# Optimization experiments

Measured on AMD Instinct MI355X. Metric: run time of the kernel, lower is better.

The kernel has to match this reference:

```python
import jax, jax.numpy as jnp
import numpy as np

B, S, H = 2, 2048, 4096
NH, HD = 32, 128  # n_heads, head_dim


def setup_inputs() -> dict:
    key = jax.random.key(0)
    ks = jax.random.split(key, 6)
    hidden_states = jax.random.normal(ks[0], (B, S, H), dtype=jnp.float32)
    alibi = jax.random.normal(ks[1], (B, NH, 1, S), dtype=jnp.float32)
    w_qkv = jax.random.normal(ks[2], (H, NH, 3 * HD), dtype=jnp.float32) * 0.02
    b_qkv = jax.random.normal(ks[3], (NH, 3 * HD), dtype=jnp.float32) * 0.02
    w_out = jax.random.normal(ks[4], (NH, HD, H), dtype=jnp.float32) * 0.02
    b_out = jax.random.normal(ks[5], (H,), dtype=jnp.float32) * 0.02
    attention_mask = jnp.ones((B, S), dtype=jnp.int32)
    return {"hidden_states": hidden_states, "alibi": alibi, "w_qkv": w_qkv,
            "b_qkv": b_qkv, "w_out": w_out, "b_out": b_out,
            "attention_mask": attention_mask}


def reference(hidden_states, alibi, w_qkv, b_qkv, w_out, b_out, attention_mask):
    dtype = hidden_states.dtype
    b, s, _ = hidden_states.shape
    # fused QKV projection: [b, s, heads, 3*head_dim]
    fused_qkv = jnp.einsum('bse,ehf->bshf', hidden_states, w_qkv) + b_qkv
    query, key, value = jnp.split(fused_qkv, 3, axis=-1)  # each [b, s, h, d]
    # causal mask fused with padding mask -> [b, 1, q, k] bool
    causal = jnp.tril(jnp.ones((s, s), dtype=bool))[None, None]
    pad = (attention_mask > 0)[:, None, None, :]
    mask = causal & pad
    mask_value = jnp.finfo(dtype).min
    attention_bias = jnp.where(mask, jnp.zeros((), dtype), jnp.full((), mask_value, dtype))
    attention_bias = attention_bias + alibi  # broadcast [b,1,q,k]+[b,h,1,k] -> [b,h,q,k]
    # scaled dot-product attention weights (query scaled by 1/sqrt(head_dim))
    scale = jnp.asarray(1.0 / np.sqrt(HD), dtype)
    scores = jnp.einsum('bqhd,bkhd->bhqk', query * scale, key) + attention_bias
    attn_weights = jax.nn.softmax(scores, axis=-1)
    attn_output = jnp.einsum('bhqk,bkhd->bqhd', attn_weights, value)
    # output projection contracting (heads, head_dim)
    out = jnp.einsum('bqhd,hde->bqe', attn_output, w_out) + b_out
    return out
```

## Files before the change

kernel.cpp:

```cpp
#include <hip/hip_runtime.h>
#include <math.h>

typedef __attribute__((ext_vector_type(8))) short bf16x8;
typedef __attribute__((ext_vector_type(4))) float f32x4;

#define MFMA16(a, b, c) __builtin_amdgcn_mfma_f32_16x16x32_bf16(a, b, c, 0, 0, 0)

#define GLD_LDS16(g, l)                                                          \
    __builtin_amdgcn_global_load_lds(                                            \
        (const __attribute__((address_space(1))) unsigned int*)(g),              \
        (__attribute__((address_space(3))) unsigned int*)(l), 16, 0, 0)

__device__ __forceinline__ short f2bf(float f) {
    union { float f; unsigned int u; } v; v.f = f;
    unsigned int u = v.u;
    u += 0x7FFFu + ((u >> 16) & 1u);
    return (short)(u >> 16);
}

__device__ __forceinline__ short f2bf_trunc(float f) {
    union { float f; unsigned int u; } v; v.f = f;
    return (short)(v.u >> 16);
}

__device__ __forceinline__ float fexp2(float x) {
#if __has_builtin(__builtin_amdgcn_exp2f)
    return __builtin_amdgcn_exp2f(x);
#else
    return __expf(x * 0.6931471805599453f);
#endif
}

__global__ __launch_bounds__(256) void cvt_kernel(const float* __restrict__ src,
                                                  short* __restrict__ dst, int n4) {
    int i = blockIdx.x * 256 + threadIdx.x;
    if (i >= n4) return;
    float4 v = ((const float4*)src)[i];
    short4 o;
    o.x = f2bf(v.x); o.y = f2bf(v.y); o.z = f2bf(v.z); o.w = f2bf(v.w);
    ((short4*)dst)[i] = o;
}

__global__ __launch_bounds__(256) void bias_prep_kernel(const float* __restrict__ alibi,
                                                        const int* __restrict__ amask,
                                                        float* __restrict__ cb) {
    int i = blockIdx.x * 256 + threadIdx.x;
    int bh = i >> 11, k = i & 2047;
    int b = bh >> 5;
    cb[i] = (amask[b * 2048 + k] > 0) ? alibi[i] * 1.4426950408889634f : -3.0e38f;
}

__global__ __launch_bounds__(256) void transpose_cvt_kernel(const float* __restrict__ src,
                                                            short* __restrict__ dst,
                                                            int R, int C) {
    __shared__ short tile[32][33];
    const int t = threadIdx.x;
    const int r0 = blockIdx.y << 5, c0 = blockIdx.x << 5;
    {
        int tr = t >> 3, tc = (t & 7) << 2;
        float4 v = *(const float4*)(src + (size_t)(r0 + tr) * C + c0 + tc);
        tile[tr][tc + 0] = f2bf(v.x);
        tile[tr][tc + 1] = f2bf(v.y);
        tile[tr][tc + 2] = f2bf(v.z);
        tile[tr][tc + 3] = f2bf(v.w);
    }
    __syncthreads();
    {
        int on = t >> 3, ok = (t & 7) << 2;
        short4 o;
        o.x = tile[ok + 0][on]; o.y = tile[ok + 1][on];
        o.z = tile[ok + 2][on]; o.w = tile[ok + 3][on];
        *(short4*)(dst + (size_t)(c0 + on) * R + r0 + ok) = o;
    }
}

__global__ __launch_bounds__(256) void qkv_gemm_kernel(const short* __restrict__ A,
                                                       const short* __restrict__ Bt,
                                                       const float* __restrict__ bias,
                                                       short* __restrict__ Qo,
                                                       short* __restrict__ Ko,
                                                       short* __restrict__ Vo) {
    const int K = 4096;
    __shared__ short As[128][32];
    __shared__ short Bs[128][32];
    const int t = threadIdx.x;
    const int m0 = blockIdx.x << 7;
    const int n0 = blockIdx.y << 7;
    const int lane = t & 63;
    const int w = t >> 6;
    const int l16 = lane & 15;
    const int quad = lane >> 4;
    const int wm = (w >> 1) << 6;
    const int wn = (w & 1) << 6;

    const int srow0 = (w << 5) + (lane >> 2);
    const int srow1 = srow0 + 16;
    const int scol = (lane & 3) << 3;

    f32x4 acc[4][4];
#pragma unroll
    for (int i = 0; i < 4; ++i)
#pragma unroll
        for (int j = 0; j < 4; ++j) acc[i][j] = (f32x4){0.f, 0.f, 0.f, 0.f};

    for (int k0 = 0; k0 < K; k0 += 32) {
        __syncthreads();
        GLD_LDS16(A + (size_t)(m0 + srow0) * K + k0 + scol, &As[srow0 & ~15][0]);
        GLD_LDS16(A + (size_t)(m0 + srow1) * K + k0 + scol, &As[srow1 & ~15][0]);
        GLD_LDS16(Bt + (size_t)(n0 + srow0) * K + k0 + scol, &Bs[srow0 & ~15][0]);
        GLD_LDS16(Bt + (size_t)(n0 + srow1) * K + k0 + scol, &Bs[srow1 & ~15][0]);
        __syncthreads();
        bf16x8 af[4], bfr[4];
#pragma unroll
        for (int mb = 0; mb < 4; ++mb)
            af[mb] = *(const bf16x8*)&As[wm + (mb << 4) + l16][quad << 3];
#pragma unroll
        for (int nb = 0; nb < 4; ++nb)
            bfr[nb] = *(const bf16x8*)&Bs[wn + (nb << 4) + l16][quad << 3];
#pragma unroll
        for (int mb = 0; mb < 4; ++mb)
#pragma unroll
            for (int nb = 0; nb < 4; ++nb)
                acc[mb][nb] = MFMA16(af[mb], bfr[nb], acc[mb][nb]);
    }

    const float qscale = 0.12751740806338946f;
#pragma unroll
    for (int nb = 0; nb < 4; ++nb) {
        int gn = n0 + wn + (nb << 4) + l16;
        float bv = bias[gn];
        int head = gn / 384, f = gn - head * 384;
#pragma unroll
        for (int mb = 0; mb < 4; ++mb) {
#pragma unroll
            for (int r = 0; r < 4; ++r) {
                int gm = m0 + wm + (mb << 4) + (quad << 2) + r;
                float v = acc[mb][nb][r] + bv;
                int b = gm >> 11, s = gm & 2047;
                int bhh = (b << 5) + head;
                if (f < 128) {
                    Qo[((size_t)bhh * 2048 + s) * 128 + f] = f2bf(v * qscale);
                } else if (f < 256) {
                    Ko[((size_t)bhh * 2048 + s) * 128 + (f - 128)] = f2bf(v);
                } else {
                    Vo[((size_t)bhh * 128 + (f - 256)) * 2048 + s] = f2bf(v);
                }
            }
        }
    }
}

__global__ __launch_bounds__(256) void out_gemm_kernel(const short* __restrict__ A,
                                                       const short* __restrict__ Bt,
                                                       const float* __restrict__ bias,
                                                       float* __restrict__ Co) {
    const int K = 4096, N = 4096;
    __shared__ short As[128][32];
    __shared__ short Bs[128][32];
    const int t = threadIdx.x;
    const int m0 = blockIdx.x << 7;
    const int n0 = blockIdx.y << 7;
    const int lane = t & 63;
    const int w = t >> 6;
    const int l16 = lane & 15;
    const int quad = lane >> 4;
    const int wm = (w >> 1) << 6;
    const int wn = (w & 1) << 6;

    const int srow0 = (w << 5) + (lane >> 2);
    const int srow1 = srow0 + 16;
    const int scol = (lane & 3) << 3;

    f32x4 acc[4][4];
#pragma unroll
    for (int i = 0; i < 4; ++i)
#pragma unroll
        for (int j = 0; j < 4; ++j) acc[i][j] = (f32x4){0.f, 0.f, 0.f, 0.f};

    for (int k0 = 0; k0 < K; k0 += 32) {
        __syncthreads();
        GLD_LDS16(A + (size_t)(m0 + srow0) * K + k0 + scol, &As[srow0 & ~15][0]);
        GLD_LDS16(A + (size_t)(m0 + srow1) * K + k0 + scol, &As[srow1 & ~15][0]);
        GLD_LDS16(Bt + (size_t)(n0 + srow0) * K + k0 + scol, &Bs[srow0 & ~15][0]);
        GLD_LDS16(Bt + (size_t)(n0 + srow1) * K + k0 + scol, &Bs[srow1 & ~15][0]);
        __syncthreads();
        bf16x8 af[4], bfr[4];
#pragma unroll
        for (int mb = 0; mb < 4; ++mb)
            af[mb] = *(const bf16x8*)&As[wm + (mb << 4) + l16][quad << 3];
#pragma unroll
        for (int nb = 0; nb < 4; ++nb)
            bfr[nb] = *(const bf16x8*)&Bs[wn + (nb << 4) + l16][quad << 3];
#pragma unroll
        for (int mb = 0; mb < 4; ++mb)
#pragma unroll
            for (int nb = 0; nb < 4; ++nb)
                acc[mb][nb] = MFMA16(af[mb], bfr[nb], acc[mb][nb]);
    }

#pragma unroll
    for (int nb = 0; nb < 4; ++nb) {
        int gn = n0 + wn + (nb << 4) + l16;
        float bv = bias[gn];
#pragma unroll
        for (int mb = 0; mb < 4; ++mb) {
#pragma unroll
            for (int r = 0; r < 4; ++r) {
                int gm = m0 + wm + (mb << 4) + (quad << 2) + r;
                Co[(size_t)gm * N + gn] = acc[mb][nb][r] + bv;
            }
        }
    }
}

__global__ __launch_bounds__(256) void attn_kernel(const short* __restrict__ Q,
                                                   const short* __restrict__ Kt,
                                                   const short* __restrict__ Vt,
                                                   const float* __restrict__ cbias,
                                                   short* __restrict__ Ot) {
    __shared__ short Ks[64][132];
    __shared__ short Vs[144][68];
    __shared__ short Ps[4][16][68];
    const int t = threadIdx.x;
    const int w = t >> 6;
    const int lane = t & 63;
    const int l16 = lane & 15;
    const int quad = lane >> 4;
    const int qt = 31 - blockIdx.x;
    const int bh = blockIdx.y;
    const int b = bh >> 5;
    const int h = bh & 31;
    const int q0t = qt << 6;

    const short* Qp = Q + (size_t)bh * 2048 * 128;
    const short* Kp = Kt + (size_t)bh * 2048 * 128;
    const short* Vp = Vt + (size_t)bh * 128 * 2048;
    const float* cb = cbias + (size_t)bh * 2048;

    const int kr = t >> 4, kc = (t & 15) << 3;
    const int vr = t >> 3, vc = (t & 7) << 3;

    for (int idx = t; idx < 16 * 68; idx += 256) {
        int rr = idx / 68, cc = idx - rr * 68;
        Vs[128 + rr][cc] = (rr == 0 && cc < 64) ? (short)0x3F80 : (short)0;
    }

    bf16x8 aq[4];
    const int myq = q0t + (w << 4) + l16;
#pragma unroll
    for (int kd = 0; kd < 4; ++kd)
        aq[kd] = *(const bf16x8*)(Qp + (size_t)myq * 128 + (kd << 5) + (quad << 3));

    f32x4 acc[9];
#pragma unroll
    for (int c = 0; c < 9; ++c) acc[c] = (f32x4){0.f, 0.f, 0.f, 0.f};
    float mrow[4];
#pragma unroll
    for (int r = 0; r < 4; ++r) mrow[r] = -3.0e38f;

    const int ktiles = qt + 1;

    bf16x8 Kreg[4], Vreg[4];
#pragma unroll
    for (int i = 0; i < 4; ++i) {
        Kreg[i] = *(const bf16x8*)(Kp + (size_t)(kr + (i << 4)) * 128 + kc);
        Vreg[i] = *(const bf16x8*)(Vp + (size_t)(vr + (i << 5)) * 2048 + vc);
    }

    for (int kt = 0; kt < ktiles; ++kt) {
        const int kk = kt << 6;
        __syncthreads();
#pragma unroll
        for (int i = 0; i < 4; ++i) {
            *(bf16x8*)&Ks[kr + (i << 4)][kc] = Kreg[i];
            *(bf16x8*)&Vs[vr + (i << 5)][vc] = Vreg[i];
        }
        if (kt + 1 < ktiles) {
            const int nk = kk + 64;
#pragma unroll
            for (int i = 0; i < 4; ++i) {
                Kreg[i] = *(const bf16x8*)(Kp + (size_t)(nk + kr + (i << 4)) * 128 + kc);
                Vreg[i] = *(const bf16x8*)(Vp + (size_t)(vr + (i << 5)) * 2048 + nk + vc);
            }
        }
        __syncthreads();

        float biasv[4];
#pragma unroll
        for (int j = 0; j < 4; ++j)
            biasv[j] = cb[kk + (j << 4) + l16];

        f32x4 sf[4];
#pragma unroll
        for (int nb = 0; nb < 4; ++nb) {
            sf[nb] = (f32x4){0.f, 0.f, 0.f, 0.f};
#pragma unroll
            for (int kd = 0; kd < 4; ++kd) {
                bf16x8 bk = *(const bf16x8*)&Ks[(nb << 4) + l16][(kd << 5) + (quad << 3)];
                sf[nb] = MFMA16(aq[kd], bk, sf[nb]);
            }
        }

        const int qrb = q0t + (w << 4) + (quad << 2);
        const bool diag = (kt == ktiles - 1);
        float alpha[4];
#pragma unroll
        for (int r = 0; r < 4; ++r) {
            float s[4];
#pragma unroll
            for (int j = 0; j < 4; ++j) s[j] = sf[j][r] + biasv[j];
            if (diag) {
                int qr = qrb + r;
#pragma unroll
                for (int j = 0; j < 4; ++j)
                    if (kk + (j << 4) + l16 > qr) s[j] = -3.0e38f;
            }
            float mx = fmaxf(fmaxf(s[0], s[1]), fmaxf(s[2], s[3]));
            mx = fmaxf(mx, __shfl_xor(mx, 1));
            mx = fmaxf(mx, __shfl_xor(mx, 2));
            mx = fmaxf(mx, __shfl_xor(mx, 4));
            mx = fmaxf(mx, __shfl_xor(mx, 8));
            float mnew = fmaxf(mrow[r], mx);
            alpha[r] = fexp2(mrow[r] - mnew);
            mrow[r] = mnew;
            int pq = (quad << 2) + r;
#pragma unroll
            for (int j = 0; j < 4; ++j)
                Ps[w][pq][(j << 4) + l16] = f2bf_trunc(fexp2(s[j] - mnew));
        }

        bf16x8 ap0 = *(const bf16x8*)&Ps[w][l16][quad << 3];
        bf16x8 ap1 = *(const bf16x8*)&Ps[w][l16][32 + (quad << 3)];
#pragma unroll
        for (int c = 0; c < 9; ++c) {
            bf16x8 bv0 = *(const bf16x8*)&Vs[(c << 4) + l16][quad << 3];
            bf16x8 bv1 = *(const bf16x8*)&Vs[(c << 4) + l16][32 + (quad << 3)];
            f32x4 ac = acc[c];
            ac[0] *= alpha[0]; ac[1] *= alpha[1]; ac[2] *= alpha[2]; ac[3] *= alpha[3];
            ac = MFMA16(ap0, bv0, ac);
            acc[c] = MFMA16(ap1, bv1, ac);
        }
    }

    float inv[4];
#pragma unroll
    for (int r = 0; r < 4; ++r) {
        float l = __shfl(acc[8][r], quad << 4);
        inv[r] = (l > 0.f) ? 1.0f / l : 0.f;
    }
    const int qbase = q0t + (w << 4) + (quad << 2);
#pragma unroll
    for (int c = 0; c < 8; ++c) {
        int d = (c << 4) + l16;
#pragma unroll
        for (int r = 0; r < 4; ++r) {
            int q = qbase + r;
            Ot[(size_t)(b * 2048 + q) * 4096 + h * 128 + d] = f2bf(acc[c][r] * inv[r]);
        }
    }
}

extern "C" void kernel_launch(void* const* d_in, const int* in_sizes, int n_in,
                              void* d_out, int out_size, void* d_ws, size_t ws_size,
                              hipStream_t stream) {
    const float* hidden = (const float*)d_in[0];
    const float* alibi  = (const float*)d_in[1];
    const float* w_qkv  = (const float*)d_in[2];
    const float* b_qkv  = (const float*)d_in[3];
    const float* w_out  = (const float*)d_in[4];
    const float* b_out  = (const float*)d_in[5];
    const int*   amask  = (const int*)d_in[6];
    float* out = (float*)d_out;

    char* ws = (char*)d_ws;
    short* hid_bf = (short*)(ws);
    short* wqkv_t = (short*)(ws + 33554432ull);
    short* wout_t = wqkv_t;
    float* cbias  = (float*)(ws + 67108864ull);
    short* Qb     = (short*)(ws + 134217728ull);
    short* Kb     = (short*)(ws + 167772160ull);
    short* Vb     = (short*)(ws + 201326592ull);
    short* attn_o = hid_bf;

    cvt_kernel<<<16384, 256, 0, stream>>>(hidden, hid_bf, 4194304);
    transpose_cvt_kernel<<<dim3(384, 128), 256, 0, stream>>>(w_qkv, wqkv_t, 4096, 12288);
    qkv_gemm_kernel<<<dim3(32, 96), 256, 0, stream>>>(hid_bf, wqkv_t, b_qkv, Qb, Kb, Vb);
    bias_prep_kernel<<<512, 256, 0, stream>>>(alibi, amask, cbias);
    transpose_cvt_kernel<<<dim3(128, 128), 256, 0, stream>>>(w_out, wout_t, 4096, 4096);
    attn_kernel<<<dim3(32, 64), 256, 0, stream>>>(Qb, Kb, Vb, cbias, attn_o);
    out_gemm_kernel<<<dim3(32, 32), 256, 0, stream>>>(attn_o, wout_t, b_out, out);
}
```

Measured before the change: 1.386 ms.

## Rewrite QKV and output GEMMs with 256x256 tiles and 4-stage LDS pipeline

Both projection GEMMs move from 128x128 tiles with 256 threads and single-buffered LDS to 256x256 tiles with 512 threads, 8 waves in a 2x4 arrangement. They also gain a 4-deep ring of global-to-LDS async loads with explicit vmcnt waits and split barriers. The LDS layout is XOR-swizzled to avoid bank conflicts, and MFMA blocks are wrapped in setprio. The goal is to hide global load latency, raise arithmetic intensity per block, and cut the two syncthreads per k-step. The cost is much higher register use (128 accumulator floats per lane), 128KB of LDS per block, and fewer blocks in flight (768 and 256).

```diff
diff --git a/kernel.cpp b/kernel.cpp
--- a/kernel.cpp
+++ b/kernel.cpp
@@ -74,68 +74,105 @@
     }
 }
 
-__global__ __launch_bounds__(256) void qkv_gemm_kernel(const short* __restrict__ A,
-                                                       const short* __restrict__ Bt,
-                                                       const float* __restrict__ bias,
-                                                       short* __restrict__ Qo,
-                                                       short* __restrict__ Ko,
-                                                       short* __restrict__ Vo) {
-    const int K = 4096;
-    __shared__ short As[128][32];
-    __shared__ short Bs[128][32];
+__global__ __launch_bounds__(512, 2) void qkv_gemm_kernel(const short* __restrict__ A,
+                                                          const short* __restrict__ Bt,
+                                                          const float* __restrict__ bias,
+                                                          short* __restrict__ Qo,
+                                                          short* __restrict__ Ko,
+                                                          short* __restrict__ Vo) {
+    __shared__ __attribute__((aligned(16))) short Al[4][8192];
+    __shared__ __attribute__((aligned(16))) short Bl[4][8192];
     const int t = threadIdx.x;
-    const int m0 = blockIdx.x << 7;
-    const int n0 = blockIdx.y << 7;
     const int lane = t & 63;
     const int w = t >> 6;
+    const int wm = w >> 2;
+    const int wn = w & 3;
     const int l16 = lane & 15;
     const int quad = lane >> 4;
-    const int wm = (w >> 1) << 6;
-    const int wn = (w & 1) << 6;
-
-    const int srow0 = (w << 5) + (lane >> 2);
-    const int srow1 = srow0 + 16;
-    const int scol = (lane & 3) << 3;
-
-    f32x4 acc[4][4];
-#pragma unroll
-    for (int i = 0; i < 4; ++i)
+    const int m0 = blockIdx.x << 8;
+    const int n0 = blockIdx.y << 8;
+
+    const int srow = lane >> 2;
+    const int skoff = (((lane & 3) ^ ((lane >> 3) & 3)) << 3);
+    const short* pA0 = A + (size_t)(m0 + (w << 5) + srow) * 4096 + skoff;
+    const short* pA1 = pA0 + (size_t)16 * 4096;
+    const short* pB0 = Bt + (size_t)(n0 + (w << 5) + srow) * 4096 + skoff;
+    const short* pB1 = pB0 + (size_t)16 * 4096;
+
+    const int qs = quad ^ ((l16 >> 1) & 3);
+    const int aoff = ((wm << 7) + l16) * 32 + (qs << 3);
+    const int boff = ((wn << 6) + l16) * 32 + (qs << 3);
+
+    f32x4 acc[8][4];
+#pragma unroll
+    for (int i = 0; i < 8; ++i)
 #pragma unroll
         for (int j = 0; j < 4; ++j) acc[i][j] = (f32x4){0.f, 0.f, 0.f, 0.f};
 
-    for (int k0 = 0; k0 < K; k0 += 32) {
-        __syncthreads();
-        GLD_LDS16(A + (size_t)(m0 + srow0) * K + k0 + scol, &As[srow0 & ~15][0]);
-        GLD_LDS16(A + (size_t)(m0 + srow1) * K + k0 + scol, &As[srow1 & ~15][0]);
-        GLD_LDS16(Bt + (size_t)(n0 + srow0) * K + k0 + scol, &Bs[srow0 & ~15][0]);
-        GLD_LDS16(Bt + (size_t)(n0 + srow1) * K + k0 + scol, &Bs[srow1 & ~15][0]);
-        __syncthreads();
-        bf16x8 af[4], bfr[4];
-#pragma unroll
-        for (int mb = 0; mb < 4; ++mb)
-            af[mb] = *(const bf16x8*)&As[wm + (mb << 4) + l16][quad << 3];
-#pragma unroll
-        for (int nb = 0; nb < 4; ++nb)
-            bfr[nb] = *(const bf16x8*)&Bs[wn + (nb << 4) + l16][quad << 3];
-#pragma unroll
-        for (int mb = 0; mb < 4; ++mb)
-#pragma unroll
-            for (int nb = 0; nb < 4; ++nb)
-                acc[mb][nb] = MFMA16(af[mb], bfr[nb], acc[mb][nb]);
-    }
+#define STAGE_A(tt) do {                                                   \
+        GLD_LDS16(pA0 + (size_t)(tt) * 32, &Al[(tt) & 3][w << 10]);        \
+        GLD_LDS16(pA1 + (size_t)(tt) * 32, &Al[(tt) & 3][(w << 10) + 512]);\
+    } while (0)
+#define STAGE_B(tt) do {                                                   \
+        GLD_LDS16(pB0 + (size_t)(tt) * 32, &Bl[(tt) & 3][w << 10]);        \
+        GLD_LDS16(pB1 + (size_t)(tt) * 32, &Bl[(tt) & 3][(w << 10) + 512]);\
+    } while (0)
+
+    STAGE_A(0); STAGE_B(0);
+    STAGE_A(1); STAGE_B(1);
+    STAGE_A(2); STAGE_B(2);
+    asm volatile("s_waitcnt vmcnt(8)" ::: "memory");
+    __builtin_amdgcn_s_barrier();
+    __builtin_amdgcn_sched_barrier(0);
+
+    for (int kt = 0; kt < 128; ++kt) {
+        const short* ab = &Al[kt & 3][0];
+        const short* bb = &Bl[kt & 3][0];
+        bf16x8 bfr[4], afr[4];
+#pragma unroll
+        for (int j = 0; j < 4; ++j) bfr[j] = *(const bf16x8*)(bb + boff + (j << 9));
+#pragma unroll
+        for (int i = 0; i < 4; ++i) afr[i] = *(const bf16x8*)(ab + aoff + (i << 9));
+        if (kt < 125) STAGE_A(kt + 3);
+        __builtin_amdgcn_s_setprio(1);
+#pragma unroll
+        for (int i = 0; i < 4; ++i)
+#pragma unroll
+            for (int j = 0; j < 4; ++j) acc[i][j] = MFMA16(afr[i], bfr[j], acc[i][j]);
+        __builtin_amdgcn_s_setprio(0);
+        __builtin_amdgcn_s_barrier();
+#pragma unroll
+        for (int i = 0; i < 4; ++i) afr[i] = *(const bf16x8*)(ab + aoff + ((i + 4) << 9));
+        if (kt < 125) STAGE_B(kt + 3);
+        __builtin_amdgcn_s_setprio(1);
+#pragma unroll
+        for (int i = 0; i < 4; ++i)
+#pragma unroll
+            for (int j = 0; j < 4; ++j) acc[i + 4][j] = MFMA16(afr[i], bfr[j], acc[i + 4][j]);
+        __builtin_amdgcn_s_setprio(0);
+        if (kt < 125)       { asm volatile("s_waitcnt vmcnt(8)" ::: "memory"); }
+        else if (kt == 125) { asm volatile("s_waitcnt vmcnt(4)" ::: "memory"); }
+        else if (kt == 126) { asm volatile("s_waitcnt vmcnt(0)" ::: "memory"); }
+        if (kt < 127) {
+            __builtin_amdgcn_s_barrier();
+            __builtin_amdgcn_sched_barrier(0);
+        }
+    }
+#undef STAGE_A
+#undef STAGE_B
 
     const float qscale = 0.12751740806338946f;
 #pragma unroll
-    for (int nb = 0; nb < 4; ++nb) {
-        int gn = n0 + wn + (nb << 4) + l16;
+    for (int j = 0; j < 4; ++j) {
+        int gn = n0 + (wn << 6) + (j << 4) + l16;
         float bv = bias[gn];
         int head = gn / 384, f = gn - head * 384;
 #pragma unroll
-        for (int mb = 0; mb < 4; ++mb) {
+        for (int i = 0; i < 8; ++i) {
 #pragma unroll
             for (int r = 0; r < 4; ++r) {
-                int gm = m0 + wm + (mb << 4) + (quad << 2) + r;
-                float v = acc[mb][nb][r] + bv;
+                int gm = m0 + (wm << 7) + (i << 4) + (quad << 2) + r;
+                float v = acc[i][j][r] + bv;
                 int b = gm >> 11, s = gm & 2047;
                 int bhh = (b << 5) + head;
                 if (f < 128) {
@@ -150,64 +187,101 @@
     }
 }
 
-__global__ __launch_bounds__(256) void out_gemm_kernel(const short* __restrict__ A,
-                                                       const short* __restrict__ Bt,
-                                                       const float* __restrict__ bias,
-                                                       float* __restrict__ Co) {
-    const int K = 4096, N = 4096;
-    __shared__ short As[128][32];
-    __shared__ short Bs[128][32];
+__global__ __launch_bounds__(512, 2) void out_gemm_kernel(const short* __restrict__ A,
+                                                          const short* __restrict__ Bt,
+                                                          const float* __restrict__ bias,
+                                                          float* __restrict__ Co) {
+    __shared__ __attribute__((aligned(16))) short Al[4][8192];
+    __shared__ __attribute__((aligned(16))) short Bl[4][8192];
     const int t = threadIdx.x;
-    const int m0 = blockIdx.x << 7;
-    const int n0 = blockIdx.y << 7;
     const int lane = t & 63;
     const int w = t >> 6;
+    const int wm = w >> 2;
+    const int wn = w & 3;
     const int l16 = lane & 15;
     const int quad = lane >> 4;
-    const int wm = (w >> 1) << 6;
-    const int wn = (w & 1) << 6;
-
-    const int srow0 = (w << 5) + (lane >> 2);
-    const int srow1 = srow0 + 16;
-    const int scol = (lane & 3) << 3;
-
-    f32x4 acc[4][4];
-#pragma unroll
-    for (int i = 0; i < 4; ++i)
+    const int m0 = blockIdx.x << 8;
+    const int n0 = blockIdx.y << 8;
+
+    const int srow = lane >> 2;
+    const int skoff = (((lane & 3) ^ ((lane >> 3) & 3)) << 3);
+    const short* pA0 = A + (size_t)(m0 + (w << 5) + srow) * 4096 + skoff;
+    const short* pA1 = pA0 + (size_t)16 * 4096;
+    const short* pB0 = Bt + (size_t)(n0 + (w << 5) + srow) * 4096 + skoff;
+    const short* pB1 = pB0 + (size_t)16 * 4096;
+
+    const int qs = quad ^ ((l16 >> 1) & 3);
+    const int aoff = ((wm << 7) + l16) * 32 + (qs << 3);
+    const int boff = ((wn << 6) + l16) * 32 + (qs << 3);
+
+    f32x4 acc[8][4];
+#pragma unroll
+    for (int i = 0; i < 8; ++i)
 #pragma unroll
         for (int j = 0; j < 4; ++j) acc[i][j] = (f32x4){0.f, 0.f, 0.f, 0.f};
 
-    for (int k0 = 0; k0 < K; k0 += 32) {
-        __syncthreads();
-        GLD_LDS16(A + (size_t)(m0 + srow0) * K + k0 + scol, &As[srow0 & ~15][0]);
-        GLD_LDS16(A + (size_t)(m0 + srow1) * K + k0 + scol, &As[srow1 & ~15][0]);
-        GLD_LDS16(Bt + (size_t)(n0 + srow0) * K + k0 + scol, &Bs[srow0 & ~15][0]);
-        GLD_LDS16(Bt + (size_t)(n0 + srow1) * K + k0 + scol, &Bs[srow1 & ~15][0]);
-        __syncthreads();
-        bf16x8 af[4], bfr[4];
-#pragma unroll
-        for (int mb = 0; mb < 4; ++mb)
-            af[mb] = *(const bf16x8*)&As[wm + (mb << 4) + l16][quad << 3];
-#pragma unroll
-        for (int nb = 0; nb < 4; ++nb)
-            bfr[nb] = *(const bf16x8*)&Bs[wn + (nb << 4) + l16][quad << 3];
-#pragma unroll
-        for (int mb = 0; mb < 4; ++mb)
-#pragma unroll
-            for (int nb = 0; nb < 4; ++nb)
-                acc[mb][nb] = MFMA16(af[mb], bfr[nb], acc[mb][nb]);
-    }
-
-#pragma unroll
-    for (int nb = 0; nb < 4; ++nb) {
-        int gn = n0 + wn + (nb << 4) + l16;
+#define STAGE_A(tt) do {                                                   \
+        GLD_LDS16(pA0 + (size_t)(tt) * 32, &Al[(tt) & 3][w << 10]);        \
+        GLD_LDS16(pA1 + (size_t)(tt) * 32, &Al[(tt) & 3][(w << 10) + 512]);\
+    } while (0)
+#define STAGE_B(tt) do {                                                   \
+        GLD_LDS16(pB0 + (size_t)(tt) * 32, &Bl[(tt) & 3][w << 10]);        \
+        GLD_LDS16(pB1 + (size_t)(tt) * 32, &Bl[(tt) & 3][(w << 10) + 512]);\
+    } while (0)
+
+    STAGE_A(0); STAGE_B(0);
+    STAGE_A(1); STAGE_B(1);
+    STAGE_A(2); STAGE_B(2);
+    asm volatile("s_waitcnt vmcnt(8)" ::: "memory");
+    __builtin_amdgcn_s_barrier();
+    __builtin_amdgcn_sched_barrier(0);
+
+    for (int kt = 0; kt < 128; ++kt) {
+        const short* ab = &Al[kt & 3][0];
+        const short* bb = &Bl[kt & 3][0];
+        bf16x8 bfr[4], afr[4];
+#pragma unroll
+        for (int j = 0; j < 4; ++j) bfr[j] = *(const bf16x8*)(bb + boff + (j << 9));
+#pragma unroll
+        for (int i = 0; i < 4; ++i) afr[i] = *(const bf16x8*)(ab + aoff + (i << 9));
+        if (kt < 125) STAGE_A(kt + 3);
+        __builtin_amdgcn_s_setprio(1);
+#pragma unroll
+        for (int i = 0; i < 4; ++i)
+#pragma unroll
+            for (int j = 0; j < 4; ++j) acc[i][j] = MFMA16(afr[i], bfr[j], acc[i][j]);
+        __builtin_amdgcn_s_setprio(0);
+        __builtin_amdgcn_s_barrier();
+#pragma unroll
+        for (int i = 0; i < 4; ++i) afr[i] = *(const bf16x8*)(ab + aoff + ((i + 4) << 9));
+        if (kt < 125) STAGE_B(kt + 3);
+        __builtin_amdgcn_s_setprio(1);
+#pragma unroll
+        for (int i = 0; i < 4; ++i)
+#pragma unroll
+            for (int j = 0; j < 4; ++j) acc[i + 4][j] = MFMA16(afr[i], bfr[j], acc[i + 4][j]);
+        __builtin_amdgcn_s_setprio(0);
+        if (kt < 125)       { asm volatile("s_waitcnt vmcnt(8)" ::: "memory"); }
+        else if (kt == 125) { asm volatile("s_waitcnt vmcnt(4)" ::: "memory"); }
+        else if (kt == 126) { asm volatile("s_waitcnt vmcnt(0)" ::: "memory"); }
+        if (kt < 127) {
+            __builtin_amdgcn_s_barrier();
+            __builtin_amdgcn_sched_barrier(0);
+        }
+    }
+#undef STAGE_A
+#undef STAGE_B
+
+#pragma unroll
+    for (int j = 0; j < 4; ++j) {
+        int gn = n0 + (wn << 6) + (j << 4) + l16;
         float bv = bias[gn];
 #pragma unroll
-        for (int mb = 0; mb < 4; ++mb) {
+        for (int i = 0; i < 8; ++i) {
 #pragma unroll
             for (int r = 0; r < 4; ++r) {
-                int gm = m0 + wm + (mb << 4) + (quad << 2) + r;
-                Co[(size_t)gm * N + gn] = acc[mb][nb][r] + bv;
+                int gm = m0 + (wm << 7) + (i << 4) + (quad << 2) + r;
+                Co[(size_t)gm * 4096 + gn] = acc[i][j][r] + bv;
             }
         }
     }
@@ -384,9 +458,9 @@
 
     cvt_kernel<<<16384, 256, 0, stream>>>(hidden, hid_bf, 4194304);
     transpose_cvt_kernel<<<dim3(384, 128), 256, 0, stream>>>(w_qkv, wqkv_t, 4096, 12288);
-    qkv_gemm_kernel<<<dim3(32, 96), 256, 0, stream>>>(hid_bf, wqkv_t, b_qkv, Qb, Kb, Vb);
+    qkv_gemm_kernel<<<dim3(16, 48), 512, 0, stream>>>(hid_bf, wqkv_t, b_qkv, Qb, Kb, Vb);
     bias_prep_kernel<<<512, 256, 0, stream>>>(alibi, amask, cbias);
     transpose_cvt_kernel<<<dim3(128, 128), 256, 0, stream>>>(w_out, wout_t, 4096, 4096);
     attn_kernel<<<dim3(32, 64), 256, 0, stream>>>(Qb, Kb, Vb, cbias, attn_o);
-    out_gemm_kernel<<<dim3(32, 32), 256, 0, stream>>>(attn_o, wout_t, b_out, out);
-}
+    out_gemm_kernel<<<dim3(16, 16), 512, 0, stream>>>(attn_o, wout_t, b_out, out);
+}
```

Result: faster. 1.236 ms (-10.8%).
